# Kernel optimization log

Measured on AMD Instinct MI355X. Metric: run time of the kernel, lower is better.

## Reference

```python
import jax, jax.numpy as jnp
import numpy as np

N_NODES = 50000
N_EDGES = 800000
D = 64  # out_dim


def setup_inputs() -> dict:
    key = jax.random.key(0)
    ks = jax.random.split(key, 9)
    K_h = jax.random.normal(ks[0], (N_NODES, D), dtype=jnp.float32)
    Q_h = jax.random.normal(ks[1], (N_NODES, D), dtype=jnp.float32)
    P_e = jax.random.normal(ks[2], (N_NODES, D), dtype=jnp.float32)
    src = jax.random.randint(ks[3], (N_EDGES,), 0, N_NODES, dtype=jnp.int32)
    dst = jax.random.randint(ks[4], (N_EDGES,), 0, N_NODES, dtype=jnp.int32)
    # MLP params: Linear(D, D) -> ReLU -> Linear(D, 1)
    lim1 = 1.0 / np.sqrt(D)
    W1 = jax.random.uniform(ks[5], (D, D), minval=-lim1, maxval=lim1, dtype=jnp.float32)
    b1 = jax.random.uniform(ks[6], (D,), minval=-lim1, maxval=lim1, dtype=jnp.float32)
    W2 = jax.random.uniform(ks[7], (D, 1), minval=-lim1, maxval=lim1, dtype=jnp.float32)
    b2 = jax.random.uniform(ks[8], (1,), minval=-lim1, maxval=lim1, dtype=jnp.float32)
    return {"K_h": K_h, "Q_h": Q_h, "P_e": P_e, "src": src, "dst": dst,
            "W1": W1, "b1": b1, "W2": W2, "b2": b2}


def reference(K_h, Q_h, P_e, src, dst, W1, b1, W2, b2):
    # Per-edge gather: src node K_h and P_e, dst node Q_h -> [E, D]
    dif = K_h[src] - Q_h[dst] + P_e[src]
    # Tiny 2-layer MLP per edge: [E, D] -> [E, D] -> [E, 1]
    h = jax.nn.relu(dif @ W1 + b1)
    score = h @ W2 + b2  # [E, 1]
    return score
```

## Files before the change

### kernel.cpp

```cpp
#include <hip/hip_runtime.h>
#include <hip/hip_fp16.h>

#define DD 64
#define NPB 64
#define LP 72

typedef _Float16 f16x8 __attribute__((ext_vector_type(8)));
typedef float    f32x4 __attribute__((ext_vector_type(4)));

__global__ __launch_bounds__(256) void node_transform_mfma(
    const float* __restrict__ K_h, const float* __restrict__ Q_h,
    const float* __restrict__ P_e, const float* __restrict__ W1,
    const float* __restrict__ b1, __half* __restrict__ A,
    __half* __restrict__ Bm, int n_nodes)
{
    __shared__ __half XH [NPB][LP];
    __shared__ __half QH [NPB][LP];
    __shared__ __half W1T[DD][LP];

    const int tid   = threadIdx.x;
    const int nbase = blockIdx.x * NPB;

    {
        const int k  = tid >> 2;
        const int n0 = (tid & 3) << 4;
        const float* wr = W1 + k * DD + n0;
        float4 w0 = *(const float4*)(wr);
        float4 w1v = *(const float4*)(wr + 4);
        float4 w2v = *(const float4*)(wr + 8);
        float4 w3v = *(const float4*)(wr + 12);
        const float wv[16] = {w0.x,w0.y,w0.z,w0.w, w1v.x,w1v.y,w1v.z,w1v.w,
                              w2v.x,w2v.y,w2v.z,w2v.w, w3v.x,w3v.y,w3v.z,w3v.w};
#pragma unroll
        for (int j = 0; j < 16; ++j)
            W1T[n0 + j][k] = __float2half(wv[j]);
    }

#pragma unroll
    for (int ch = 0; ch < 4; ++ch) {
        int idx = tid + (ch << 8);
        int r   = idx >> 4;
        int q4  = idx & 15;
        int node = nbase + r;
        float4 kv = make_float4(0.f,0.f,0.f,0.f);
        float4 pv = kv, qv = kv;
        if (node < n_nodes) {
            kv = *(const float4*)(K_h + (size_t)node * DD + q4 * 4);
            pv = *(const float4*)(P_e + (size_t)node * DD + q4 * 4);
            qv = *(const float4*)(Q_h + (size_t)node * DD + q4 * 4);
        }
        __half2* xh = (__half2*)&XH[r][q4 << 2];
        xh[0] = __float22half2_rn(make_float2(kv.x + pv.x, kv.y + pv.y));
        xh[1] = __float22half2_rn(make_float2(kv.z + pv.z, kv.w + pv.w));
        __half2* qh = (__half2*)&QH[r][q4 << 2];
        qh[0] = __float22half2_rn(make_float2(qv.x, qv.y));
        qh[1] = __float22half2_rn(make_float2(qv.z, qv.w));
    }
    __syncthreads();

    const int w    = tid >> 6;
    const int lane = tid & 63;
    const int m    = lane & 15;
    const int q    = lane >> 4;
    const int row  = (w << 4) + m;

    f16x8 xlo = *(const f16x8*)&XH[row][(q << 3)];
    f16x8 xhi = *(const f16x8*)&XH[row][32 + (q << 3)];
    f16x8 qlo = *(const f16x8*)&QH[row][(q << 3)];
    f16x8 qhi = *(const f16x8*)&QH[row][32 + (q << 3)];

    f32x4 accA[4], accB[4];
#pragma unroll
    for (int t = 0; t < 4; ++t) {
        float bb = b1[t * 16 + m];
        accA[t] = (f32x4){bb, bb, bb, bb};
        accB[t] = (f32x4){0.f, 0.f, 0.f, 0.f};
        f16x8 wlo = *(const f16x8*)&W1T[t * 16 + m][(q << 3)];
        f16x8 whi = *(const f16x8*)&W1T[t * 16 + m][32 + (q << 3)];
        accA[t] = __builtin_amdgcn_mfma_f32_16x16x32_f16(xlo, wlo, accA[t], 0, 0, 0);
        accA[t] = __builtin_amdgcn_mfma_f32_16x16x32_f16(xhi, whi, accA[t], 0, 0, 0);
        accB[t] = __builtin_amdgcn_mfma_f32_16x16x32_f16(qlo, wlo, accB[t], 0, 0, 0);
        accB[t] = __builtin_amdgcn_mfma_f32_16x16x32_f16(qhi, whi, accB[t], 0, 0, 0);
    }

#pragma unroll
    for (int r = 0; r < 4; ++r) {
        int node = nbase + (w << 4) + (q << 2) + r;
        if (node >= n_nodes) continue;
        __half* Arow = A  + (size_t)node * DD + m;
        __half* Brow = Bm + (size_t)node * DD + m;
#pragma unroll
        for (int t = 0; t < 4; ++t) {
            Arow[t * 16] = __float2half(accA[t][r]);
            Brow[t * 16] = __float2half(accB[t][r]);
        }
    }
}

__global__ __launch_bounds__(256) void edge_score_kernel(
    const __half* __restrict__ A, const __half* __restrict__ Bm,
    const int* __restrict__ src, const int* __restrict__ dst,
    const float* __restrict__ W2, const float* __restrict__ b2,
    float* __restrict__ out, int n_edges)
{
    const int tid = threadIdx.x;
    const int g   = tid >> 3;
    const int c   = tid & 7;
    const int e0  = (blockIdx.x << 7) + (g << 2);
    if (e0 >= n_edges) return;

    float4 w0 = *(const float4*)(W2 + c * 8);
    float4 w1 = *(const float4*)(W2 + c * 8 + 4);
    const float wv[8] = {w0.x, w0.y, w0.z, w0.w, w1.x, w1.y, w1.z, w1.w};
    const size_t coff = (size_t)(c * 8);

    if (e0 + 3 < n_edges) {
        int4 sv = *(const int4*)(src + e0);
        int4 dv = *(const int4*)(dst + e0);

        float4 ra0 = *(const float4*)(A  + (size_t)sv.x * DD + coff);
        float4 rb0 = *(const float4*)(Bm + (size_t)dv.x * DD + coff);
        float4 ra1 = *(const float4*)(A  + (size_t)sv.y * DD + coff);
        float4 rb1 = *(const float4*)(Bm + (size_t)dv.y * DD + coff);
        float4 ra2 = *(const float4*)(A  + (size_t)sv.z * DD + coff);
        float4 rb2 = *(const float4*)(Bm + (size_t)dv.z * DD + coff);
        float4 ra3 = *(const float4*)(A  + (size_t)sv.w * DD + coff);
        float4 rb3 = *(const float4*)(Bm + (size_t)dv.w * DD + coff);

        float acc0 = 0.f, acc1 = 0.f, acc2 = 0.f, acc3 = 0.f;
        const __half2* ah0 = (const __half2*)&ra0;
        const __half2* bh0 = (const __half2*)&rb0;
        const __half2* ah1 = (const __half2*)&ra1;
        const __half2* bh1 = (const __half2*)&rb1;
        const __half2* ah2 = (const __half2*)&ra2;
        const __half2* bh2 = (const __half2*)&rb2;
        const __half2* ah3 = (const __half2*)&ra3;
        const __half2* bh3 = (const __half2*)&rb3;
#pragma unroll
        for (int j = 0; j < 4; ++j) {
            float2 x, y;
            x = __half22float2(ah0[j]); y = __half22float2(bh0[j]);
            acc0 = fmaf(fmaxf(x.x - y.x, 0.f), wv[2 * j + 0], acc0);
            acc0 = fmaf(fmaxf(x.y - y.y, 0.f), wv[2 * j + 1], acc0);
            x = __half22float2(ah1[j]); y = __half22float2(bh1[j]);
            acc1 = fmaf(fmaxf(x.x - y.x, 0.f), wv[2 * j + 0], acc1);
            acc1 = fmaf(fmaxf(x.y - y.y, 0.f), wv[2 * j + 1], acc1);
            x = __half22float2(ah2[j]); y = __half22float2(bh2[j]);
            acc2 = fmaf(fmaxf(x.x - y.x, 0.f), wv[2 * j + 0], acc2);
            acc2 = fmaf(fmaxf(x.y - y.y, 0.f), wv[2 * j + 1], acc2);
            x = __half22float2(ah3[j]); y = __half22float2(bh3[j]);
            acc3 = fmaf(fmaxf(x.x - y.x, 0.f), wv[2 * j + 0], acc3);
            acc3 = fmaf(fmaxf(x.y - y.y, 0.f), wv[2 * j + 1], acc3);
        }

        acc0 += __shfl_xor(acc0, 1); acc1 += __shfl_xor(acc1, 1);
        acc2 += __shfl_xor(acc2, 1); acc3 += __shfl_xor(acc3, 1);
        acc0 += __shfl_xor(acc0, 2); acc1 += __shfl_xor(acc1, 2);
        acc2 += __shfl_xor(acc2, 2); acc3 += __shfl_xor(acc3, 2);
        acc0 += __shfl_xor(acc0, 4); acc1 += __shfl_xor(acc1, 4);
        acc2 += __shfl_xor(acc2, 4); acc3 += __shfl_xor(acc3, 4);

        if (c == 0) {
            float bb = b2[0];
            *(float4*)(out + e0) =
                make_float4(acc0 + bb, acc1 + bb, acc2 + bb, acc3 + bb);
        }
    } else {
        for (int e = e0; e < n_edges && e < e0 + 4; ++e) {
            int s = src[e], d = dst[e];
            float4 ar = *(const float4*)(A  + (size_t)s * DD + coff);
            float4 br = *(const float4*)(Bm + (size_t)d * DD + coff);
            const __half2* ah = (const __half2*)&ar;
            const __half2* bh = (const __half2*)&br;
            float acc = 0.f;
#pragma unroll
            for (int j = 0; j < 4; ++j) {
                float2 x = __half22float2(ah[j]);
                float2 y = __half22float2(bh[j]);
                acc = fmaf(fmaxf(x.x - y.x, 0.f), wv[2 * j + 0], acc);
                acc = fmaf(fmaxf(x.y - y.y, 0.f), wv[2 * j + 1], acc);
            }
            acc += __shfl_xor(acc, 1);
            acc += __shfl_xor(acc, 2);
            acc += __shfl_xor(acc, 4);
            if (c == 0) out[e] = acc + b2[0];
        }
    }
}

extern "C" void kernel_launch(void* const* d_in, const int* in_sizes, int n_in,
                              void* d_out, int out_size, void* d_ws, size_t ws_size,
                              hipStream_t stream) {
    const float* K_h = (const float*)d_in[0];
    const float* Q_h = (const float*)d_in[1];
    const float* P_e = (const float*)d_in[2];
    const int*   src = (const int*)d_in[3];
    const int*   dst = (const int*)d_in[4];
    const float* W1  = (const float*)d_in[5];
    const float* b1  = (const float*)d_in[6];
    const float* W2  = (const float*)d_in[7];
    const float* b2  = (const float*)d_in[8];
    float* out = (float*)d_out;

    int n_nodes = in_sizes[0] / DD;
    int n_edges = in_sizes[3];

    __half* A  = (__half*)d_ws;
    __half* Bm = A + (size_t)n_nodes * DD;

    node_transform_mfma<<<(n_nodes + NPB - 1) / NPB, 256, 0, stream>>>(
        K_h, Q_h, P_e, W1, b1, A, Bm, n_nodes);
    edge_score_kernel<<<(n_edges + 127) / 128, 256, 0, stream>>>(
        A, Bm, src, dst, W2, b2, out, n_edges);
}
```

Baseline: 121.3 us.

## Make edge kernel grid-stride persistent with software-prefetched edge indices

The edge scoring kernel becomes a grid-stride loop over groups of four edges, with the grid capped at 2048 blocks instead of one block per 128 edges. Each iteration loads the next group's src/dst indices while the current group's gathers and reduction run, so index-load latency overlaps with work. This also amortises the per-block W2 and b2 loads. The cost is fewer resident blocks to hide random-gather latency, plus extra registers for the prefetched indices.

```diff
diff --git a/kernel.cpp b/kernel.cpp
--- a/kernel.cpp
+++ b/kernel.cpp
@@ -106,85 +106,107 @@
     const int tid = threadIdx.x;
     const int g   = tid >> 3;
     const int c   = tid & 7;
-    const int e0  = (blockIdx.x << 7) + (g << 2);
-    if (e0 >= n_edges) return;
+    const int ngroups = (n_edges + 3) >> 2;
+    const int gstride = gridDim.x << 5;
 
     float4 w0 = *(const float4*)(W2 + c * 8);
     float4 w1 = *(const float4*)(W2 + c * 8 + 4);
     const float wv[8] = {w0.x, w0.y, w0.z, w0.w, w1.x, w1.y, w1.z, w1.w};
+    const float bb = b2[0];
     const size_t coff = (size_t)(c * 8);
 
-    if (e0 + 3 < n_edges) {
-        int4 sv = *(const int4*)(src + e0);
-        int4 dv = *(const int4*)(dst + e0);
-
-        float4 ra0 = *(const float4*)(A  + (size_t)sv.x * DD + coff);
-        float4 rb0 = *(const float4*)(Bm + (size_t)dv.x * DD + coff);
-        float4 ra1 = *(const float4*)(A  + (size_t)sv.y * DD + coff);
-        float4 rb1 = *(const float4*)(Bm + (size_t)dv.y * DD + coff);
-        float4 ra2 = *(const float4*)(A  + (size_t)sv.z * DD + coff);
-        float4 rb2 = *(const float4*)(Bm + (size_t)dv.z * DD + coff);
-        float4 ra3 = *(const float4*)(A  + (size_t)sv.w * DD + coff);
-        float4 rb3 = *(const float4*)(Bm + (size_t)dv.w * DD + coff);
-
-        float acc0 = 0.f, acc1 = 0.f, acc2 = 0.f, acc3 = 0.f;
-        const __half2* ah0 = (const __half2*)&ra0;
-        const __half2* bh0 = (const __half2*)&rb0;
-        const __half2* ah1 = (const __half2*)&ra1;
-        const __half2* bh1 = (const __half2*)&rb1;
-        const __half2* ah2 = (const __half2*)&ra2;
-        const __half2* bh2 = (const __half2*)&rb2;
-        const __half2* ah3 = (const __half2*)&ra3;
-        const __half2* bh3 = (const __half2*)&rb3;
-#pragma unroll
-        for (int j = 0; j < 4; ++j) {
-            float2 x, y;
-            x = __half22float2(ah0[j]); y = __half22float2(bh0[j]);
-            acc0 = fmaf(fmaxf(x.x - y.x, 0.f), wv[2 * j + 0], acc0);
-            acc0 = fmaf(fmaxf(x.y - y.y, 0.f), wv[2 * j + 1], acc0);
-            x = __half22float2(ah1[j]); y = __half22float2(bh1[j]);
-            acc1 = fmaf(fmaxf(x.x - y.x, 0.f), wv[2 * j + 0], acc1);
-            acc1 = fmaf(fmaxf(x.y - y.y, 0.f), wv[2 * j + 1], acc1);
-            x = __half22float2(ah2[j]); y = __half22float2(bh2[j]);
-            acc2 = fmaf(fmaxf(x.x - y.x, 0.f), wv[2 * j + 0], acc2);
-            acc2 = fmaf(fmaxf(x.y - y.y, 0.f), wv[2 * j + 1], acc2);
-            x = __half22float2(ah3[j]); y = __half22float2(bh3[j]);
-            acc3 = fmaf(fmaxf(x.x - y.x, 0.f), wv[2 * j + 0], acc3);
-            acc3 = fmaf(fmaxf(x.y - y.y, 0.f), wv[2 * j + 1], acc3);
+    int gid = (blockIdx.x << 5) + g;
+
+    int4 sv = make_int4(0, 0, 0, 0), dv = sv;
+    if (gid < ngroups && (gid << 2) + 3 < n_edges) {
+        sv = *(const int4*)(src + (gid << 2));
+        dv = *(const int4*)(dst + (gid << 2));
+    }
+
+    while (gid < ngroups) {
+        const int e0 = gid << 2;
+        const int gid_next = gid + gstride;
+
+        if (e0 + 3 < n_edges) {
+            float4 ra0 = *(const float4*)(A  + (size_t)sv.x * DD + coff);
+            float4 rb0 = *(const float4*)(Bm + (size_t)dv.x * DD + coff);
+            float4 ra1 = *(const float4*)(A  + (size_t)sv.y * DD + coff);
+            float4 rb1 = *(const float4*)(Bm + (size_t)dv.y * DD + coff);
+            float4 ra2 = *(const float4*)(A  + (size_t)sv.z * DD + coff);
+            float4 rb2 = *(const float4*)(Bm + (size_t)dv.z * DD + coff);
+            float4 ra3 = *(const float4*)(A  + (size_t)sv.w * DD + coff);
+            float4 rb3 = *(const float4*)(Bm + (size_t)dv.w * DD + coff);
+
+            int4 svn = make_int4(0, 0, 0, 0), dvn = svn;
+            if (gid_next < ngroups && (gid_next << 2) + 3 < n_edges) {
+                svn = *(const int4*)(src + (gid_next << 2));
+                dvn = *(const int4*)(dst + (gid_next << 2));
+            }
+
+            float acc0 = 0.f, acc1 = 0.f, acc2 = 0.f, acc3 = 0.f;
+            const __half2* ah0 = (const __half2*)&ra0;
+            const __half2* bh0 = (const __half2*)&rb0;
+            const __half2* ah1 = (const __half2*)&ra1;
+            const __half2* bh1 = (const __half2*)&rb1;
+            const __half2* ah2 = (const __half2*)&ra2;
+            const __half2* bh2 = (const __half2*)&rb2;
+            const __half2* ah3 = (const __half2*)&ra3;
+            const __half2* bh3 = (const __half2*)&rb3;
+#pragma unroll
+            for (int j = 0; j < 4; ++j) {
+                float2 x, y;
+                x = __half22float2(ah0[j]); y = __half22float2(bh0[j]);
+                acc0 = fmaf(fmaxf(x.x - y.x, 0.f), wv[2 * j + 0], acc0);
+                acc0 = fmaf(fmaxf(x.y - y.y, 0.f), wv[2 * j + 1], acc0);
+                x = __half22float2(ah1[j]); y = __half22float2(bh1[j]);
+                acc1 = fmaf(fmaxf(x.x - y.x, 0.f), wv[2 * j + 0], acc1);
+                acc1 = fmaf(fmaxf(x.y - y.y, 0.f), wv[2 * j + 1], acc1);
+                x = __half22float2(ah2[j]); y = __half22float2(bh2[j]);
+                acc2 = fmaf(fmaxf(x.x - y.x, 0.f), wv[2 * j + 0], acc2);
+                acc2 = fmaf(fmaxf(x.y - y.y, 0.f), wv[2 * j + 1], acc2);
+                x = __half22float2(ah3[j]); y = __half22float2(bh3[j]);
+                acc3 = fmaf(fmaxf(x.x - y.x, 0.f), wv[2 * j + 0], acc3);
+                acc3 = fmaf(fmaxf(x.y - y.y, 0.f), wv[2 * j + 1], acc3);
+            }
+
+            acc0 += __shfl_xor(acc0, 1); acc1 += __shfl_xor(acc1, 1);
+            acc2 += __shfl_xor(acc2, 1); acc3 += __shfl_xor(acc3, 1);
+            acc0 += __shfl_xor(acc0, 2); acc1 += __shfl_xor(acc1, 2);
+            acc2 += __shfl_xor(acc2, 2); acc3 += __shfl_xor(acc3, 2);
+            acc0 += __shfl_xor(acc0, 4); acc1 += __shfl_xor(acc1, 4);
+            acc2 += __shfl_xor(acc2, 4); acc3 += __shfl_xor(acc3, 4);
+
+            if (c == 0) {
+                *(float4*)(out + e0) =
+                    make_float4(acc0 + bb, acc1 + bb, acc2 + bb, acc3 + bb);
+            }
+            sv = svn; dv = dvn;
+        } else {
+            for (int e = e0; e < n_edges; ++e) {
+                int s = src[e], d = dst[e];
+                float4 ar = *(const float4*)(A  + (size_t)s * DD + coff);
+                float4 br = *(const float4*)(Bm + (size_t)d * DD + coff);
+                const __half2* ah = (const __half2*)&ar;
+                const __half2* bh = (const __half2*)&br;
+                float acc = 0.f;
+#pragma unroll
+                for (int j = 0; j < 4; ++j) {
+                    float2 x = __half22float2(ah[j]);
+                    float2 y = __half22float2(bh[j]);
+                    acc = fmaf(fmaxf(x.x - y.x, 0.f), wv[2 * j + 0], acc);
+                    acc = fmaf(fmaxf(x.y - y.y, 0.f), wv[2 * j + 1], acc);
+                }
+                acc += __shfl_xor(acc, 1);
+                acc += __shfl_xor(acc, 2);
+                acc += __shfl_xor(acc, 4);
+                if (c == 0) out[e] = acc + bb;
+            }
+            if (gid_next < ngroups && (gid_next << 2) + 3 < n_edges) {
+                sv = *(const int4*)(src + (gid_next << 2));
+                dv = *(const int4*)(dst + (gid_next << 2));
+            }
         }
-
-        acc0 += __shfl_xor(acc0, 1); acc1 += __shfl_xor(acc1, 1);
-        acc2 += __shfl_xor(acc2, 1); acc3 += __shfl_xor(acc3, 1);
-        acc0 += __shfl_xor(acc0, 2); acc1 += __shfl_xor(acc1, 2);
-        acc2 += __shfl_xor(acc2, 2); acc3 += __shfl_xor(acc3, 2);
-        acc0 += __shfl_xor(acc0, 4); acc1 += __shfl_xor(acc1, 4);
-        acc2 += __shfl_xor(acc2, 4); acc3 += __shfl_xor(acc3, 4);
-
-        if (c == 0) {
-            float bb = b2[0];
-            *(float4*)(out + e0) =
-                make_float4(acc0 + bb, acc1 + bb, acc2 + bb, acc3 + bb);
-        }
-    } else {
-        for (int e = e0; e < n_edges && e < e0 + 4; ++e) {
-            int s = src[e], d = dst[e];
-            float4 ar = *(const float4*)(A  + (size_t)s * DD + coff);
-            float4 br = *(const float4*)(Bm + (size_t)d * DD + coff);
-            const __half2* ah = (const __half2*)&ar;
-            const __half2* bh = (const __half2*)&br;
-            float acc = 0.f;
-#pragma unroll
-            for (int j = 0; j < 4; ++j) {
-                float2 x = __half22float2(ah[j]);
-                float2 y = __half22float2(bh[j]);
-                acc = fmaf(fmaxf(x.x - y.x, 0.f), wv[2 * j + 0], acc);
-                acc = fmaf(fmaxf(x.y - y.y, 0.f), wv[2 * j + 1], acc);
-            }
-            acc += __shfl_xor(acc, 1);
-            acc += __shfl_xor(acc, 2);
-            acc += __shfl_xor(acc, 4);
-            if (c == 0) out[e] = acc + b2[0];
-        }
+        gid = gid_next;
     }
 }
 
@@ -210,6 +232,10 @@
 
     node_transform_mfma<<<(n_nodes + NPB - 1) / NPB, 256, 0, stream>>>(
         K_h, Q_h, P_e, W1, b1, A, Bm, n_nodes);
-    edge_score_kernel<<<(n_edges + 127) / 128, 256, 0, stream>>>(
+
+    int ngroups = (n_edges + 3) >> 2;
+    int nblocks = (ngroups + 31) / 32;
+    if (nblocks > 2048) nblocks = 2048;
+    edge_score_kernel<<<nblocks, 256, 0, stream>>>(
         A, Bm, src, dst, W2, b2, out, n_edges);
 }
```

After: 122.6 us. Within noise of the previous version (+1.1%).
